# Kernel optimization log

Hardware: AMD Instinct MI355X
Metric: run time of the kernel (lower is better)

Reference implementation:

```python
import jax, jax.numpy as jnp
import numpy as np

N, B, PER, NELEM, E = 8192, 32, 256, 5, 131072
H, F, G, L = 128, 128, 50, 6
NC = B * NELEM
CUTOFF = 10.0
LOG2 = float(np.log(2.0))


def ssp(x):
    return jax.nn.softplus(x) - LOG2


def setup_inputs() -> dict:
    key = jax.random.key(0)
    ks = jax.random.split(key, 24)
    pos = jax.random.normal(ks[0], (N, 3), dtype=jnp.float32) * 2.0
    # component structure: node n in graph g gets element slot n % NELEM
    comp_id = (jnp.arange(N) // PER) * NELEM + (jnp.arange(N) % NELEM)
    comps_z = jax.random.randint(ks[1], (NC,), 1, 100)
    z = comps_z[comp_id]
    # edges restricted to within a graph (mimics radius_graph with batch)
    eg = jax.random.randint(ks[2], (E,), 0, B)
    src = eg * PER + jax.random.randint(ks[3], (E,), 0, PER)
    dst = eg * PER + jax.random.randint(ks[4], (E,), 0, PER)
    edge_index = jnp.stack([src, dst], axis=0)
    s = 0.05
    p = lambda k, shp: jax.random.normal(k, shp, dtype=jnp.float32) * s
    return {
        "pos": pos,
        "emb_table": p(ks[5], (100, H)),
        "mlp_w1": p(ks[6], (L, G, F)),
        "mlp_b1": jnp.zeros((L, F), jnp.float32),
        "mlp_w2": p(ks[7], (L, F, F)),
        "mlp_b2": jnp.zeros((L, F), jnp.float32),
        "cf_lin1_w": p(ks[8], (L, H, F)),
        "cf_lin2_w": p(ks[9], (L, F, H)),
        "cf_lin2_b": jnp.zeros((L, H), jnp.float32),
        "int_lin_w": p(ks[10], (L, H, H)),
        "int_lin_b": jnp.zeros((L, H), jnp.float32),
        "out_w1": p(ks[11], (H, H // 2)),
        "out_b1": jnp.zeros((H // 2,), jnp.float32),
        "out_w2": p(ks[12], (H // 2, 1)),
        "out_b2": jnp.zeros((1,), jnp.float32),
        "z": z,
        "comp_id": comp_id,
        "edge_index": edge_index,
        "comps_z": comps_z,
    }


def reference(pos, emb_table, mlp_w1, mlp_b1, mlp_w2, mlp_b2,
              cf_lin1_w, cf_lin2_w, cf_lin2_b, int_lin_w, int_lin_b,
              out_w1, out_b1, out_w2, out_b2,
              z, comp_id, edge_index, comps_z):
    src, dst = edge_index[0], edge_index[1]
    # edge distances and Gaussian smearing
    ew = jnp.linalg.norm(pos[src] - pos[dst], axis=-1)              # [E]
    offset = jnp.linspace(0.0, CUTOFF, G)
    coeff = -0.5 / (offset[1] - offset[0]) ** 2
    edge_attr = jnp.exp(coeff * (ew[:, None] - offset[None, :]) ** 2)  # [E,G]
    # cutoff envelope used by CFConv
    C = CUTOFF / (1e-10 + ew ** 2) - 1.0                            # [E]

    h = emb_table[z]                 # [N,H] node features (fixed across blocks)
    types = emb_table[comps_z]       # [NC,H] component features

    counts = jax.ops.segment_sum(jnp.ones((N,), jnp.float32), comp_id,
                                 num_segments=NC)                   # [NC]
    batch_c = jnp.arange(NC) // NELEM

    for i in range(L):
        # edge filter MLP * cutoff weight
        W = ssp(edge_attr @ mlp_w1[i] + mlp_b1[i]) @ mlp_w2[i] + mlp_b2[i]
        W = W * C[:, None]                                          # [E,F]
        xh = h @ cf_lin1_w[i]                                       # [N,F]
        msg = xh[src] * W                                           # [E,F]
        agg = jax.ops.segment_sum(msg, dst, num_segments=N)         # [N,F]
        # per-component mean pooling
        comp = jax.ops.segment_sum(agg, comp_id, num_segments=NC) / counts[:, None]
        x = comp @ cf_lin2_w[i] + cf_lin2_b[i]                      # [NC,H]
        x = ssp(x) @ int_lin_w[i] + int_lin_b[i]
        types = types + x

    # readout (num_tasks=1, n_seq=None branch)
    h2 = ssp(types @ out_w1 + out_b1)
    per_comp = h2 @ out_w2 + out_b2                                 # [NC,1]
    out = jax.ops.segment_sum(per_comp, batch_c, num_segments=B)    # [B,1]
    return out
```

## Files before the change

kernel.cpp:

```cpp
#include <hip/hip_runtime.h>


#define NNODES 8192
#define NGRAPH 32
#define NELEM  5
#define NEDGE  131072
#define HD     128
#define FD     128
#define GD     50
#define LL     6
#define NC     160
#define NZ     100
#define CUT    10.0f
#define LOG2_  0.69314718055994531f
#define LOG2E_ 1.44269504088896340f
#define QDC    0.84932181f

#define CAP    1024
#define PADE   (NC * CAP)
#define PADG   (PADE / 64)
#define GPITCH 72
#define TPITCH 136
#define CSTR   16

#define W1F_ELEMS (LL * 2 * 8 * 64 * 8)
#define W2F_ELEMS (LL * 4 * 8 * 64 * 8)
#define NSCATB   (NEDGE / 256)
#define NFRAGB   ((W1F_ELEMS + W2F_ELEMS) / 256)
#define NXHZB    (LL * NZ / 2)
#define NB2PB    3

typedef _Float16 half8 __attribute__((ext_vector_type(8)));
typedef float floatx4 __attribute__((ext_vector_type(4)));

#if __has_builtin(__builtin_amdgcn_exp2f)
#define EXP2F(x) __builtin_amdgcn_exp2f(x)
#else
#define EXP2F(x) __expf((x) * LOG2_)
#endif
#if __has_builtin(__builtin_amdgcn_logf)
#define LOG2F_(x) __builtin_amdgcn_logf(x)
#else
#define LOG2F_(x) (__logf(x) * LOG2E_)
#endif

__device__ __forceinline__ float ssp(float x) {
    float m = fmaxf(x, 0.0f);
    float z = __expf(-fabsf(x));
    return m + __logf(1.0f + z) - LOG2_;
}

__global__ __launch_bounds__(256) void setup_kernel(
    const float* __restrict__ pos, const int* __restrict__ ei,
    const int* __restrict__ comp_id, const int* __restrict__ z,
    const float* __restrict__ w1, const float* __restrict__ w2,
    const float* __restrict__ b2in,
    const float* __restrict__ emb, const float* __restrict__ cf1,
    int* __restrict__ counts, int* __restrict__ cursor,
    float* __restrict__ ew_s, float* __restrict__ c_s, int* __restrict__ zsrc_s,
    _Float16* __restrict__ w1f, _Float16* __restrict__ w2f,
    float* __restrict__ xh_z, float* __restrict__ b2p)
{
    int bx = blockIdx.x;
    int tid = threadIdx.x;
    if (bx < NSCATB) {
        int e = bx * 256 + tid;
        int s = ei[e], d = ei[NEDGE + e];
        float dx = pos[3*s]   - pos[3*d];
        float dy = pos[3*s+1] - pos[3*d+1];
        float dz = pos[3*s+2] - pos[3*d+2];
        float d2 = dx*dx + dy*dy + dz*dz;
        float ew = sqrtf(d2);
        float C  = CUT / (1e-10f + d2) - 1.0f;
        int cid = comp_id[d];
        int idx = cid * CAP + atomicAdd(&cursor[cid * CSTR], 1);
        ew_s[idx] = ew; c_s[idx] = C; zsrc_s[idx] = z[s];
        if (e < NNODES) atomicAdd(&counts[comp_id[e]], 1);
        return;
    }
    int fx = bx - NSCATB;
    if (fx < NFRAGB) {
        int idx = fx * 256 + tid;
        if (idx < W1F_ELEMS) {
            int j = idx & 7, lane = (idx >> 3) & 63, tcg = (idx >> 9) & 7;
            int kb = (idx >> 12) & 1, l = idx >> 13;
            int k = kb * 32 + (lane >> 4) * 8 + j;
            int col = tcg * 16 + (lane & 15);
            float v = (k < GD) ? w1[(l * GD + k) * FD + col] : 0.0f;
            w1f[idx] = (_Float16)(v * LOG2E_);
        } else {
            int id2 = idx - W1F_ELEMS;
            int j = id2 & 7, lane = (id2 >> 3) & 63, tcg = (id2 >> 9) & 7;
            int kb = (id2 >> 12) & 3, l = id2 >> 14;
            int k = kb * 32 + (lane >> 4) * 8 + j;
            int col = tcg * 16 + (lane & 15);
            w2f[id2] = (_Float16)(LOG2_ * w2[(l * FD + k) * FD + col]);
        }
        return;
    }
    int bz = fx - NFRAGB;
    if (bz < NXHZB) {
        int l = bz / (NZ / 2);
        int zv = (bz % (NZ / 2)) * 2 + (tid >> 7);
        int f = tid & 127;
        const float* h = emb + zv * HD;
        const float* w = cf1 + l * HD * FD;
        float acc = 0.0f;
        #pragma unroll 8
        for (int k = 0; k < HD; ++k) acc = fmaf(h[k], w[k * FD + f], acc);
        xh_z[(l * NZ + zv) * FD + f] = acc;
    } else {
        int idx2 = (bz - NXHZB) * 256 + tid;
        int l = idx2 >> 7, fo = idx2 & 127;
        float sum = 0.0f;
        #pragma unroll 8
        for (int fi = 0; fi < FD; ++fi)
            sum += (float)(_Float16)(LOG2_ * w2[(l * FD + fi) * FD + fo]);
        b2p[idx2] = b2in[l * FD + fo] - sum;
    }
}

__global__ __launch_bounds__(256, 8) void edge_kernel(
    const float* __restrict__ ew_s, const float* __restrict__ c_s,
    const int* __restrict__ zsrc_s,
    const _Float16* __restrict__ w1f, const float* __restrict__ b1_,
    const _Float16* __restrict__ w2f, const float* __restrict__ b2p_,
    const float* __restrict__ xh_z, float* __restrict__ comp_acc)
{
    __shared__ __align__(16) _Float16 smem[64 * TPITCH];
    __shared__ float ce_l[64];
    __shared__ int   zs_l[64];

    const int tid  = threadIdx.x;
    const int lane = tid & 63;
    const int l15  = lane & 15;
    const int quad = lane >> 4;
    const int fq   = __builtin_amdgcn_readfirstlane(tid >> 6);
    const int l    = blockIdx.y;
    const int cid  = blockIdx.x % NC;
    const int gg   = blockIdx.x / NC;
    const int g0   = cid * CAP + gg * 64;

    const float delta = CUT / (GD - 1);
    const float Qe = QDC / delta;

    const float ce = c_s[g0 + lane];
    if (__all(ce == 0.0f)) return;
    if (tid < 64) {
        ce_l[tid] = ce;
        zs_l[tid] = zsrc_s[g0 + tid] * (FD * 4);
    }
    const int colbase = fq * 32 + l15;
    const float b1c0 = b1_[l * FD + colbase] * LOG2E_;
    const float b1c1 = b1_[l * FD + colbase + 16] * LOG2E_;
    const float b2c0 = b2p_[l * FD + colbase];
    const float b2c1 = b2p_[l * FD + colbase + 16];

    {
        const float qewr = ew_s[g0 + lane] * Qe;
        half8 ga, gb;
        #pragma unroll
        for (int i = 0; i < 8; ++i) {
            float u0 = qewr - (fq * 16 + i) * QDC;
            float u1 = qewr - (fq * 16 + 8 + i) * QDC;
            ga[i] = (_Float16)EXP2F(-(u0 * u0));
            gb[i] = (_Float16)EXP2F(-(u1 * u1));
        }
        *(half8*)&smem[lane * GPITCH + fq * 16]     = ga;
        *(half8*)&smem[lane * GPITCH + fq * 16 + 8] = gb;
    }
    __syncthreads();

    floatx4 accT[4][2];
    #pragma unroll
    for (int tr = 0; tr < 4; ++tr) {
        accT[tr][0] = (floatx4){b1c0, b1c0, b1c0, b1c0};
        accT[tr][1] = (floatx4){b1c1, b1c1, b1c1, b1c1};
    }
    const half8* w1fp = (const half8*)w1f;
    #pragma unroll
    for (int kb = 0; kb < 2; ++kb) {
        half8 bf0 = w1fp[((l * 2 + kb) * 8 + fq * 2 + 0) * 64 + lane];
        half8 bf1 = w1fp[((l * 2 + kb) * 8 + fq * 2 + 1) * 64 + lane];
        #pragma unroll
        for (int tr = 0; tr < 4; ++tr) {
            half8 af = *(const half8*)&smem[(tr * 16 + l15) * GPITCH + kb * 32 + quad * 8];
            accT[tr][0] = __builtin_amdgcn_mfma_f32_16x16x32_f16(af, bf0, accT[tr][0], 0, 0, 0);
            accT[tr][1] = __builtin_amdgcn_mfma_f32_16x16x32_f16(af, bf1, accT[tr][1], 0, 0, 0);
        }
    }
    __syncthreads();

    #pragma unroll
    for (int tr = 0; tr < 4; ++tr) {
        #pragma unroll
        for (int tcl = 0; tcl < 2; ++tcl) {
            #pragma unroll
            for (int r = 0; r < 4; ++r) {
                float ee = EXP2F(accT[tr][tcl][r]);
                smem[(tr * 16 + quad * 4 + r) * TPITCH + fq * 32 + tcl * 16 + l15]
                    = (_Float16)LOG2F_(1.0f + ee);
            }
        }
    }
    __syncthreads();

    floatx4 accW[4][2];
    #pragma unroll
    for (int tr = 0; tr < 4; ++tr) {
        accW[tr][0] = (floatx4){b2c0, b2c0, b2c0, b2c0};
        accW[tr][1] = (floatx4){b2c1, b2c1, b2c1, b2c1};
    }
    const half8* w2fp = (const half8*)w2f;
    #pragma unroll
    for (int kb = 0; kb < 4; ++kb) {
        half8 bf0 = w2fp[((l * 4 + kb) * 8 + fq * 2 + 0) * 64 + lane];
        half8 bf1 = w2fp[((l * 4 + kb) * 8 + fq * 2 + 1) * 64 + lane];
        #pragma unroll
        for (int tr = 0; tr < 4; ++tr) {
            half8 af = *(const half8*)&smem[(tr * 16 + l15) * TPITCH + kb * 32 + quad * 8];
            accW[tr][0] = __builtin_amdgcn_mfma_f32_16x16x32_f16(af, bf0, accW[tr][0], 0, 0, 0);
            accW[tr][1] = __builtin_amdgcn_mfma_f32_16x16x32_f16(af, bf1, accW[tr][1], 0, 0, 0);
        }
    }

    const char* xb = (const char*)(xh_z + l * NZ * FD) + colbase * 4;
    float s0 = 0.0f, s1 = 0.0f;
    #pragma unroll
    for (int tr = 0; tr < 4; ++tr) {
        #pragma unroll
        for (int r = 0; r < 4; ++r) {
            const int e = tr * 16 + quad * 4 + r;
            const float cee = ce_l[e];
            const float* xr = (const float*)(xb + zs_l[e]);
            float p0 = cee * xr[0];
            float p1 = cee * xr[16];
            s0 = fmaf(accW[tr][0][r], p0, s0);
            s1 = fmaf(accW[tr][1][r], p1, s1);
        }
    }
    s0 += __shfl_xor(s0, 16); s0 += __shfl_xor(s0, 32);
    s1 += __shfl_xor(s1, 16); s1 += __shfl_xor(s1, 32);
    float* cacc = comp_acc + (l * NC + cid) * FD + fq * 32;
    if (quad == 0) {
        atomicAdd(&cacc[l15],      s0);
        atomicAdd(&cacc[l15 + 16], s1);
    }
}

__global__ __launch_bounds__(128) void comp_kernel(
    const float* __restrict__ comp_acc, const int* __restrict__ counts,
    const float* __restrict__ cf2w, const float* __restrict__ cf2b,
    const float* __restrict__ intw, const float* __restrict__ intb,
    float* __restrict__ types_acc)
{
    int c = blockIdx.x, l = blockIdx.y, f = threadIdx.x;
    __shared__ float comp[FD];
    __shared__ float sx[FD];
    comp[f] = comp_acc[(l * NC + c) * FD + f] / (float)counts[c];
    __syncthreads();
    float acc = cf2b[l * HD + f];
    const float* w = cf2w + l * FD * HD;
    #pragma unroll 8
    for (int k = 0; k < FD; ++k) acc = fmaf(comp[k], w[k * HD + f], acc);
    sx[f] = ssp(acc);
    __syncthreads();
    float acc2 = intb[l * HD + f];
    const float* wi = intw + l * HD * HD;
    #pragma unroll 8
    for (int k = 0; k < HD; ++k) acc2 = fmaf(sx[k], wi[k * HD + f], acc2);
    atomicAdd(&types_acc[c * HD + f], acc2);
}

__global__ __launch_bounds__(64) void readout_kernel(
    const float* __restrict__ types_acc, const float* __restrict__ emb,
    const int* __restrict__ comps_z,
    const float* __restrict__ w1, const float* __restrict__ b1,
    const float* __restrict__ w2, const float* __restrict__ b2,
    float* __restrict__ out)
{
    int b = blockIdx.x, lane = threadIdx.x;
    float sum = 0.0f;
    for (int cc = 0; cc < NELEM; ++cc) {
        int c = b * NELEM + cc;
        int zc = comps_z[c];
        float acc = b1[lane];
        const float* ta = types_acc + c * HD;
        const float* eb = emb + zc * HD;
        #pragma unroll 8
        for (int k = 0; k < HD; ++k) acc = fmaf(ta[k] + eb[k], w1[k * 64 + lane], acc);
        sum += ssp(acc) * w2[lane];
    }
    #pragma unroll
    for (int s = 32; s > 0; s >>= 1) sum += __shfl_xor(sum, s);
    if (lane == 0) out[b] = sum + (float)NELEM * b2[0];
}

extern "C" void kernel_launch(void* const* d_in, const int* in_sizes, int n_in,
                              void* d_out, int out_size, void* d_ws, size_t ws_size,
                              hipStream_t stream) {
    (void)in_sizes; (void)n_in; (void)out_size; (void)ws_size;
    const float* pos     = (const float*)d_in[0];
    const float* emb     = (const float*)d_in[1];
    const float* mlp_w1  = (const float*)d_in[2];
    const float* mlp_b1  = (const float*)d_in[3];
    const float* mlp_w2  = (const float*)d_in[4];
    const float* mlp_b2  = (const float*)d_in[5];
    const float* cf1     = (const float*)d_in[6];
    const float* cf2w    = (const float*)d_in[7];
    const float* cf2b    = (const float*)d_in[8];
    const float* intw    = (const float*)d_in[9];
    const float* intb    = (const float*)d_in[10];
    const float* ow1     = (const float*)d_in[11];
    const float* ob1     = (const float*)d_in[12];
    const float* ow2     = (const float*)d_in[13];
    const float* ob2     = (const float*)d_in[14];
    const int*   z       = (const int*)d_in[15];
    const int*   comp_id = (const int*)d_in[16];
    const int*   ei      = (const int*)d_in[17];
    const int*   comps_z = (const int*)d_in[18];
    float* out = (float*)d_out;

    char* ws = (char*)d_ws;
    size_t off = 0;
    auto alloc = [&](size_t bytes) -> void* {
        void* p = ws + off;
        off += (bytes + 255) & ~(size_t)255;
        return p;
    };
    float* comp_acc  = (float*)alloc((size_t)LL * NC * FD * 4);
    int*   counts    = (int*)  alloc(NC * 4);
    float* types_acc = (float*)alloc((size_t)NC * HD * 4);
    int*   cursor    = (int*)  alloc(NC * CSTR * 4);
    float* c_s       = (float*)alloc((size_t)PADE * 4);
    int*   zsrc_s    = (int*)  alloc((size_t)PADE * 4);
    size_t zero_bytes = off;
    float* ew_s     = (float*)alloc((size_t)PADE * 4);
    float* xh_z     = (float*)alloc((size_t)LL * NZ * FD * 4);
    float* b2p      = (float*)alloc((size_t)LL * FD * 4);
    _Float16* w1f   = (_Float16*)alloc((size_t)W1F_ELEMS * 2);
    _Float16* w2f   = (_Float16*)alloc((size_t)W2F_ELEMS * 2);

    hipMemsetAsync(d_ws, 0, zero_bytes, stream);

    setup_kernel<<<NSCATB + NFRAGB + NXHZB + NB2PB, 256, 0, stream>>>(
        pos, ei, comp_id, z, mlp_w1, mlp_w2, mlp_b2, emb, cf1,
        counts, cursor, ew_s, c_s, zsrc_s, w1f, w2f, xh_z, b2p);
    edge_kernel <<<dim3(PADG, LL), 256, 0, stream>>>(ew_s, c_s, zsrc_s,
                                                     w1f, mlp_b1, w2f, b2p,
                                                     xh_z, comp_acc);
    comp_kernel <<<dim3(NC, LL), 128, 0, stream>>>(comp_acc, counts, cf2w, cf2b,
                                                   intw, intb, types_acc);
    readout_kernel<<<NGRAPH, 64, 0, stream>>>(types_acc, emb, comps_z,
                                              ow1, ob1, ow2, ob2, out);
}
```

Measured before the change: 212.1 us.

## Process three layers per edge block, swizzle LDS, and pack xh_z pairs

Each edge_kernel block now loops over three layers instead of one, so the grid's y dimension drops from 6 to 2. The Gaussian smearing, the early-exit check and the per-edge metadata loads are shared across those layers. The LDS writes and reads of the hidden activations are XOR-swizzled to reduce bank conflicts. xh_z columns are permuted in setup so each lane can fetch its two features with one float2 load, and ce/zsrc are packed into one int2 in LDS. ew_s is moved into the zeroed region, which adds memset work, and the lower occupancy hint plus fewer blocks reduce the parallelism available to hide latency.

Measured after the change: 224.7 us. +5.9%, slower.

```diff
diff --git a/kernel.cpp b/kernel.cpp
--- a/kernel.cpp
+++ b/kernel.cpp
@@ -108,7 +108,8 @@
         float acc = 0.0f;
         #pragma unroll 8
         for (int k = 0; k < HD; ++k) acc = fmaf(h[k], w[k * FD + f], acc);
-        xh_z[(l * NZ + zv) * FD + f] = acc;
+        int fp = ((f >> 5) * 32) + ((f & 15) * 2) + ((f >> 4) & 1);
+        xh_z[(l * NZ + zv) * FD + fp] = acc;
     } else {
         int idx2 = (bz - NXHZB) * 256 + tid;
         int l = idx2 >> 7, fo = idx2 & 127;
@@ -120,7 +121,7 @@
     }
 }
 
-__global__ __launch_bounds__(256, 8) void edge_kernel(
+__global__ __launch_bounds__(256, 6) void edge_kernel(
     const float* __restrict__ ew_s, const float* __restrict__ c_s,
     const int* __restrict__ zsrc_s,
     const _Float16* __restrict__ w1f, const float* __restrict__ b1_,
@@ -128,37 +129,28 @@
     const float* __restrict__ xh_z, float* __restrict__ comp_acc)
 {
     __shared__ __align__(16) _Float16 smem[64 * TPITCH];
-    __shared__ float ce_l[64];
-    __shared__ int   zs_l[64];
+    __shared__ int2 cz_l[64];
 
     const int tid  = threadIdx.x;
     const int lane = tid & 63;
     const int l15  = lane & 15;
     const int quad = lane >> 4;
     const int fq   = __builtin_amdgcn_readfirstlane(tid >> 6);
-    const int l    = blockIdx.y;
     const int cid  = blockIdx.x % NC;
     const int gg   = blockIdx.x / NC;
     const int g0   = cid * CAP + gg * 64;
+    const int l0   = blockIdx.y * 3;
+
+    const float ce = c_s[g0 + lane];
+    if (__all(ce == 0.0f)) return;
+    if (tid < 64)
+        cz_l[tid] = make_int2(__float_as_int(ce), zsrc_s[g0 + tid] * (FD * 4));
 
     const float delta = CUT / (GD - 1);
     const float Qe = QDC / delta;
-
-    const float ce = c_s[g0 + lane];
-    if (__all(ce == 0.0f)) return;
-    if (tid < 64) {
-        ce_l[tid] = ce;
-        zs_l[tid] = zsrc_s[g0 + tid] * (FD * 4);
-    }
-    const int colbase = fq * 32 + l15;
-    const float b1c0 = b1_[l * FD + colbase] * LOG2E_;
-    const float b1c1 = b1_[l * FD + colbase + 16] * LOG2E_;
-    const float b2c0 = b2p_[l * FD + colbase];
-    const float b2c1 = b2p_[l * FD + colbase + 16];
-
+    half8 ga, gb;
     {
         const float qewr = ew_s[g0 + lane] * Qe;
-        half8 ga, gb;
         #pragma unroll
         for (int i = 0; i < 8; ++i) {
             float u0 = qewr - (fq * 16 + i) * QDC;
@@ -166,85 +158,101 @@
             ga[i] = (_Float16)EXP2F(-(u0 * u0));
             gb[i] = (_Float16)EXP2F(-(u1 * u1));
         }
+    }
+    const int colbase = fq * 32 + l15;
+    const int wsw = quad << 4;
+    const int rsw = ((l15 >> 2) & 3) << 4;
+
+    #pragma unroll 1
+    for (int li = 0; li < 3; ++li) {
+        const int l = l0 + li;
+
         *(half8*)&smem[lane * GPITCH + fq * 16]     = ga;
         *(half8*)&smem[lane * GPITCH + fq * 16 + 8] = gb;
-    }
-    __syncthreads();
-
-    floatx4 accT[4][2];
-    #pragma unroll
-    for (int tr = 0; tr < 4; ++tr) {
-        accT[tr][0] = (floatx4){b1c0, b1c0, b1c0, b1c0};
-        accT[tr][1] = (floatx4){b1c1, b1c1, b1c1, b1c1};
-    }
-    const half8* w1fp = (const half8*)w1f;
-    #pragma unroll
-    for (int kb = 0; kb < 2; ++kb) {
-        half8 bf0 = w1fp[((l * 2 + kb) * 8 + fq * 2 + 0) * 64 + lane];
-        half8 bf1 = w1fp[((l * 2 + kb) * 8 + fq * 2 + 1) * 64 + lane];
+        const float b1c0 = b1_[l * FD + colbase] * LOG2E_;
+        const float b1c1 = b1_[l * FD + colbase + 16] * LOG2E_;
+        const float b2c0 = b2p_[l * FD + colbase];
+        const float b2c1 = b2p_[l * FD + colbase + 16];
+        __syncthreads();
+
+        floatx4 accT[4][2];
         #pragma unroll
         for (int tr = 0; tr < 4; ++tr) {
-            half8 af = *(const half8*)&smem[(tr * 16 + l15) * GPITCH + kb * 32 + quad * 8];
-            accT[tr][0] = __builtin_amdgcn_mfma_f32_16x16x32_f16(af, bf0, accT[tr][0], 0, 0, 0);
-            accT[tr][1] = __builtin_amdgcn_mfma_f32_16x16x32_f16(af, bf1, accT[tr][1], 0, 0, 0);
-        }
-    }
-    __syncthreads();
-
-    #pragma unroll
-    for (int tr = 0; tr < 4; ++tr) {
-        #pragma unroll
-        for (int tcl = 0; tcl < 2; ++tcl) {
+            accT[tr][0] = (floatx4){b1c0, b1c0, b1c0, b1c0};
+            accT[tr][1] = (floatx4){b1c1, b1c1, b1c1, b1c1};
+        }
+        const half8* w1fp = (const half8*)w1f;
+        #pragma unroll
+        for (int kb = 0; kb < 2; ++kb) {
+            half8 bf0 = w1fp[((l * 2 + kb) * 8 + fq * 2 + 0) * 64 + lane];
+            half8 bf1 = w1fp[((l * 2 + kb) * 8 + fq * 2 + 1) * 64 + lane];
+            #pragma unroll
+            for (int tr = 0; tr < 4; ++tr) {
+                half8 af = *(const half8*)&smem[(tr * 16 + l15) * GPITCH + kb * 32 + quad * 8];
+                accT[tr][0] = __builtin_amdgcn_mfma_f32_16x16x32_f16(af, bf0, accT[tr][0], 0, 0, 0);
+                accT[tr][1] = __builtin_amdgcn_mfma_f32_16x16x32_f16(af, bf1, accT[tr][1], 0, 0, 0);
+            }
+        }
+        __syncthreads();
+
+        #pragma unroll
+        for (int tr = 0; tr < 4; ++tr) {
+            #pragma unroll
+            for (int tcl = 0; tcl < 2; ++tcl) {
+                #pragma unroll
+                for (int r = 0; r < 4; ++r) {
+                    float ee = EXP2F(accT[tr][tcl][r]);
+                    smem[(tr * 16 + quad * 4 + r) * TPITCH
+                         + ((fq * 32 + tcl * 16 + l15) ^ wsw)]
+                        = (_Float16)LOG2F_(1.0f + ee);
+                }
+            }
+        }
+        __syncthreads();
+
+        floatx4 accW[4][2];
+        #pragma unroll
+        for (int tr = 0; tr < 4; ++tr) {
+            accW[tr][0] = (floatx4){b2c0, b2c0, b2c0, b2c0};
+            accW[tr][1] = (floatx4){b2c1, b2c1, b2c1, b2c1};
+        }
+        const half8* w2fp = (const half8*)w2f;
+        #pragma unroll
+        for (int kb = 0; kb < 4; ++kb) {
+            half8 bf0 = w2fp[((l * 4 + kb) * 8 + fq * 2 + 0) * 64 + lane];
+            half8 bf1 = w2fp[((l * 4 + kb) * 8 + fq * 2 + 1) * 64 + lane];
+            #pragma unroll
+            for (int tr = 0; tr < 4; ++tr) {
+                half8 af = *(const half8*)&smem[(tr * 16 + l15) * TPITCH
+                                                + ((kb * 32 + quad * 8) ^ rsw)];
+                accW[tr][0] = __builtin_amdgcn_mfma_f32_16x16x32_f16(af, bf0, accW[tr][0], 0, 0, 0);
+                accW[tr][1] = __builtin_amdgcn_mfma_f32_16x16x32_f16(af, bf1, accW[tr][1], 0, 0, 0);
+            }
+        }
+
+        const char* xb = (const char*)xh_z
+                       + ((size_t)(l * NZ * FD) + (size_t)(fq * 32 + l15 * 2)) * 4;
+        float s0 = 0.0f, s1 = 0.0f;
+        #pragma unroll
+        for (int tr = 0; tr < 4; ++tr) {
             #pragma unroll
             for (int r = 0; r < 4; ++r) {
-                float ee = EXP2F(accT[tr][tcl][r]);
-                smem[(tr * 16 + quad * 4 + r) * TPITCH + fq * 32 + tcl * 16 + l15]
-                    = (_Float16)LOG2F_(1.0f + ee);
+                const int e = tr * 16 + quad * 4 + r;
+                int2 cz = cz_l[e];
+                float cee = __int_as_float(cz.x);
+                const float2 xr = *(const float2*)(xb + cz.y);
+                s0 = fmaf(accW[tr][0][r], cee * xr.x, s0);
+                s1 = fmaf(accW[tr][1][r], cee * xr.y, s1);
             }
         }
-    }
-    __syncthreads();
-
-    floatx4 accW[4][2];
-    #pragma unroll
-    for (int tr = 0; tr < 4; ++tr) {
-        accW[tr][0] = (floatx4){b2c0, b2c0, b2c0, b2c0};
-        accW[tr][1] = (floatx4){b2c1, b2c1, b2c1, b2c1};
-    }
-    const half8* w2fp = (const half8*)w2f;
-    #pragma unroll
-    for (int kb = 0; kb < 4; ++kb) {
-        half8 bf0 = w2fp[((l * 4 + kb) * 8 + fq * 2 + 0) * 64 + lane];
-        half8 bf1 = w2fp[((l * 4 + kb) * 8 + fq * 2 + 1) * 64 + lane];
-        #pragma unroll
-        for (int tr = 0; tr < 4; ++tr) {
-            half8 af = *(const half8*)&smem[(tr * 16 + l15) * TPITCH + kb * 32 + quad * 8];
-            accW[tr][0] = __builtin_amdgcn_mfma_f32_16x16x32_f16(af, bf0, accW[tr][0], 0, 0, 0);
-            accW[tr][1] = __builtin_amdgcn_mfma_f32_16x16x32_f16(af, bf1, accW[tr][1], 0, 0, 0);
-        }
-    }
-
-    const char* xb = (const char*)(xh_z + l * NZ * FD) + colbase * 4;
-    float s0 = 0.0f, s1 = 0.0f;
-    #pragma unroll
-    for (int tr = 0; tr < 4; ++tr) {
-        #pragma unroll
-        for (int r = 0; r < 4; ++r) {
-            const int e = tr * 16 + quad * 4 + r;
-            const float cee = ce_l[e];
-            const float* xr = (const float*)(xb + zs_l[e]);
-            float p0 = cee * xr[0];
-            float p1 = cee * xr[16];
-            s0 = fmaf(accW[tr][0][r], p0, s0);
-            s1 = fmaf(accW[tr][1][r], p1, s1);
-        }
-    }
-    s0 += __shfl_xor(s0, 16); s0 += __shfl_xor(s0, 32);
-    s1 += __shfl_xor(s1, 16); s1 += __shfl_xor(s1, 32);
-    float* cacc = comp_acc + (l * NC + cid) * FD + fq * 32;
-    if (quad == 0) {
-        atomicAdd(&cacc[l15],      s0);
-        atomicAdd(&cacc[l15 + 16], s1);
+        s0 += __shfl_xor(s0, 16); s0 += __shfl_xor(s0, 32);
+        s1 += __shfl_xor(s1, 16); s1 += __shfl_xor(s1, 32);
+        float* cacc = comp_acc + (l * NC + cid) * FD + fq * 32;
+        if (quad == 0) {
+            atomicAdd(&cacc[l15],      s0);
+            atomicAdd(&cacc[l15 + 16], s1);
+        }
+        if (li < 2) __syncthreads();
     }
 }
 
@@ -334,8 +342,8 @@
     int*   cursor    = (int*)  alloc(NC * CSTR * 4);
     float* c_s       = (float*)alloc((size_t)PADE * 4);
     int*   zsrc_s    = (int*)  alloc((size_t)PADE * 4);
+    float* ew_s      = (float*)alloc((size_t)PADE * 4);
     size_t zero_bytes = off;
-    float* ew_s     = (float*)alloc((size_t)PADE * 4);
     float* xh_z     = (float*)alloc((size_t)LL * NZ * FD * 4);
     float* b2p      = (float*)alloc((size_t)LL * FD * 4);
     _Float16* w1f   = (_Float16*)alloc((size_t)W1F_ELEMS * 2);
@@ -346,9 +354,9 @@
     setup_kernel<<<NSCATB + NFRAGB + NXHZB + NB2PB, 256, 0, stream>>>(
         pos, ei, comp_id, z, mlp_w1, mlp_w2, mlp_b2, emb, cf1,
         counts, cursor, ew_s, c_s, zsrc_s, w1f, w2f, xh_z, b2p);
-    edge_kernel <<<dim3(PADG, LL), 256, 0, stream>>>(ew_s, c_s, zsrc_s,
-                                                     w1f, mlp_b1, w2f, b2p,
-                                                     xh_z, comp_acc);
+    edge_kernel <<<dim3(PADG, 2), 256, 0, stream>>>(ew_s, c_s, zsrc_s,
+                                                    w1f, mlp_b1, w2f, b2p,
+                                                    xh_z, comp_acc);
     comp_kernel <<<dim3(NC, LL), 128, 0, stream>>>(comp_acc, counts, cf2w, cf2b,
                                                    intw, intb, types_acc);
     readout_kernel<<<NGRAPH, 64, 0, stream>>>(types_acc, emb, comps_z,
```

## Replace per-edge filter MLP with interpolated distance lookup table

Applied to the files above, without the earlier changes.

The filter network depends only on the scalar edge distance, so it is evaluated once per layer on a 2048-point distance grid in the setup kernel and stored as an fp16 table. The edge kernel then linearly interpolates table rows instead of running two MFMA matmuls per edge. It also handles all six layers in one block, sharing edge metadata and issuing fewer launches. The trade-off is interpolation and fp16 error, plus clamping of distances beyond the table range (about 12.8).

Measured after the change: 273.6 us. 1.29x slower.

```diff
diff --git a/kernel.cpp b/kernel.cpp
--- a/kernel.cpp
+++ b/kernel.cpp
@@ -13,54 +13,43 @@
 #define NZ     100
 #define CUT    10.0f
 #define LOG2_  0.69314718055994531f
-#define LOG2E_ 1.44269504088896340f
-#define QDC    0.84932181f
 
 #define CAP    1024
 #define PADE   (NC * CAP)
 #define PADG   (PADE / 64)
-#define GPITCH 72
-#define TPITCH 136
 #define CSTR   16
 
-#define W1F_ELEMS (LL * 2 * 8 * 64 * 8)
-#define W2F_ELEMS (LL * 4 * 8 * 64 * 8)
-#define NSCATB   (NEDGE / 256)
-#define NFRAGB   ((W1F_ELEMS + W2F_ELEMS) / 256)
-#define NXHZB    (LL * NZ / 2)
-#define NB2PB    3
-
-typedef _Float16 half8 __attribute__((ext_vector_type(8)));
-typedef float floatx4 __attribute__((ext_vector_type(4)));
-
-#if __has_builtin(__builtin_amdgcn_exp2f)
-#define EXP2F(x) __builtin_amdgcn_exp2f(x)
-#else
-#define EXP2F(x) __expf((x) * LOG2_)
-#endif
-#if __has_builtin(__builtin_amdgcn_logf)
-#define LOG2F_(x) __builtin_amdgcn_logf(x)
-#else
-#define LOG2F_(x) (__logf(x) * LOG2E_)
-#endif
+#define NK     2048
+#define TI     32
+#define HSTEP  0.00625f
+#define INVH   160.0f
+#define DELTA  (10.0f / 49.0f)
+#define COEFF  (-12.005f)
+
+#define NSCATB (NEDGE / 256)
+#define NXHZB  (LL * NZ / 2)
+#define NTABB  (LL * (NK / TI))
+
+typedef _Float16 h2 __attribute__((ext_vector_type(2)));
 
 __device__ __forceinline__ float ssp(float x) {
     float m = fmaxf(x, 0.0f);
-    float z = __expf(-fabsf(x));
-    return m + __logf(1.0f + z) - LOG2_;
+    float zz = __expf(-fabsf(x));
+    return m + __logf(1.0f + zz) - LOG2_;
 }
 
 __global__ __launch_bounds__(256) void setup_kernel(
     const float* __restrict__ pos, const int* __restrict__ ei,
     const int* __restrict__ comp_id, const int* __restrict__ z,
-    const float* __restrict__ w1, const float* __restrict__ w2,
-    const float* __restrict__ b2in,
+    const float* __restrict__ w1, const float* __restrict__ b1in,
+    const float* __restrict__ w2, const float* __restrict__ b2in,
     const float* __restrict__ emb, const float* __restrict__ cf1,
     int* __restrict__ counts, int* __restrict__ cursor,
     float* __restrict__ ew_s, float* __restrict__ c_s, int* __restrict__ zsrc_s,
-    _Float16* __restrict__ w1f, _Float16* __restrict__ w2f,
-    float* __restrict__ xh_z, float* __restrict__ b2p)
-{
+    _Float16* __restrict__ xh16, _Float16* __restrict__ tab)
+{
+    __shared__ float Gl[TI][52];
+    __shared__ float Sl[TI][FD];
     int bx = blockIdx.x;
     int tid = threadIdx.x;
     if (bx < NSCATB) {
@@ -78,27 +67,7 @@
         if (e < NNODES) atomicAdd(&counts[comp_id[e]], 1);
         return;
     }
-    int fx = bx - NSCATB;
-    if (fx < NFRAGB) {
-        int idx = fx * 256 + tid;
-        if (idx < W1F_ELEMS) {
-            int j = idx & 7, lane = (idx >> 3) & 63, tcg = (idx >> 9) & 7;
-            int kb = (idx >> 12) & 1, l = idx >> 13;
-            int k = kb * 32 + (lane >> 4) * 8 + j;
-            int col = tcg * 16 + (lane & 15);
-            float v = (k < GD) ? w1[(l * GD + k) * FD + col] : 0.0f;
-            w1f[idx] = (_Float16)(v * LOG2E_);
-        } else {
-            int id2 = idx - W1F_ELEMS;
-            int j = id2 & 7, lane = (id2 >> 3) & 63, tcg = (id2 >> 9) & 7;
-            int kb = (id2 >> 12) & 3, l = id2 >> 14;
-            int k = kb * 32 + (lane >> 4) * 8 + j;
-            int col = tcg * 16 + (lane & 15);
-            w2f[id2] = (_Float16)(LOG2_ * w2[(l * FD + k) * FD + col]);
-        }
-        return;
-    }
-    int bz = fx - NFRAGB;
+    int bz = bx - NSCATB;
     if (bz < NXHZB) {
         int l = bz / (NZ / 2);
         int zv = (bz % (NZ / 2)) * 2 + (tid >> 7);
@@ -108,143 +77,111 @@
         float acc = 0.0f;
         #pragma unroll 8
         for (int k = 0; k < HD; ++k) acc = fmaf(h[k], w[k * FD + f], acc);
-        xh_z[(l * NZ + zv) * FD + f] = acc;
-    } else {
-        int idx2 = (bz - NXHZB) * 256 + tid;
-        int l = idx2 >> 7, fo = idx2 & 127;
-        float sum = 0.0f;
-        #pragma unroll 8
-        for (int fi = 0; fi < FD; ++fi)
-            sum += (float)(_Float16)(LOG2_ * w2[(l * FD + fi) * FD + fo]);
-        b2p[idx2] = b2in[l * FD + fo] - sum;
+        xh16[(l * NZ + zv) * FD + f] = (_Float16)acc;
+        return;
+    }
+    int bt = bz - NXHZB;
+    int l  = bt >> 6;
+    int i0 = (bt & 63) * TI;
+    for (int idx = tid; idx < TI * GD; idx += 256) {
+        int il = idx / GD, k = idx - il * GD;
+        float d = (float)(i0 + il) * HSTEP - (float)k * DELTA;
+        Gl[il][k] = __expf(COEFF * d * d);
+    }
+    __syncthreads();
+    {
+        int f = tid & 127;
+        float b1v = b1in[l * FD + f];
+        #pragma unroll 1
+        for (int it = 0; it < TI / 2; ++it) {
+            int il = (tid >> 7) + it * 2;
+            float t = b1v;
+            #pragma unroll 10
+            for (int k = 0; k < GD; ++k)
+                t = fmaf(Gl[il][k], w1[(l * GD + k) * FD + f], t);
+            Sl[il][f] = ssp(t);
+        }
+    }
+    __syncthreads();
+    {
+        int f = tid & 127;
+        float b2v = b2in[l * FD + f];
+        #pragma unroll 1
+        for (int it = 0; it < TI / 2; ++it) {
+            int il = (tid >> 7) + it * 2;
+            float wv = b2v;
+            #pragma unroll 8
+            for (int k = 0; k < FD; ++k)
+                wv = fmaf(Sl[il][k], w2[(l * FD + k) * FD + f], wv);
+            tab[((size_t)(l * NK + i0 + il)) * FD + f] = (_Float16)wv;
+        }
     }
 }
 
 __global__ __launch_bounds__(256, 8) void edge_kernel(
     const float* __restrict__ ew_s, const float* __restrict__ c_s,
     const int* __restrict__ zsrc_s,
-    const _Float16* __restrict__ w1f, const float* __restrict__ b1_,
-    const _Float16* __restrict__ w2f, const float* __restrict__ b2p_,
-    const float* __restrict__ xh_z, float* __restrict__ comp_acc)
-{
-    __shared__ __align__(16) _Float16 smem[64 * TPITCH];
-    __shared__ float ce_l[64];
-    __shared__ int   zs_l[64];
+    const _Float16* __restrict__ tab, const _Float16* __restrict__ xh16,
+    float* __restrict__ comp_acc)
+{
+    __shared__ int4 meta[64];
 
     const int tid  = threadIdx.x;
     const int lane = tid & 63;
-    const int l15  = lane & 15;
-    const int quad = lane >> 4;
-    const int fq   = __builtin_amdgcn_readfirstlane(tid >> 6);
-    const int l    = blockIdx.y;
+    const int fq   = tid >> 6;
     const int cid  = blockIdx.x % NC;
     const int gg   = blockIdx.x / NC;
     const int g0   = cid * CAP + gg * 64;
 
-    const float delta = CUT / (GD - 1);
-    const float Qe = QDC / delta;
-
     const float ce = c_s[g0 + lane];
     if (__all(ce == 0.0f)) return;
+
     if (tid < 64) {
-        ce_l[tid] = ce;
-        zs_l[tid] = zsrc_s[g0 + tid] * (FD * 4);
-    }
-    const int colbase = fq * 32 + l15;
-    const float b1c0 = b1_[l * FD + colbase] * LOG2E_;
-    const float b1c1 = b1_[l * FD + colbase + 16] * LOG2E_;
-    const float b2c0 = b2p_[l * FD + colbase];
-    const float b2c1 = b2p_[l * FD + colbase + 16];
-
-    {
-        const float qewr = ew_s[g0 + lane] * Qe;
-        half8 ga, gb;
+        float ew = ew_s[g0 + tid];
+        int zz   = zsrc_s[g0 + tid];
+        float fi = ew * INVH;
+        int i = (int)fi; if (i > NK - 2) i = NK - 2;
+        float fr = fi - (float)i; if (fr > 1.0f) fr = 1.0f;
+        meta[tid] = make_int4(i * (FD * 2), __float_as_int(fr),
+                              __float_as_int(c_s[g0 + tid]), zz * (FD * 2));
+    }
+    __syncthreads();
+
+    float acc[LL][2];
+    #pragma unroll
+    for (int l = 0; l < LL; ++l) { acc[l][0] = 0.0f; acc[l][1] = 0.0f; }
+
+    const int lane4 = lane * 4;
+    for (int k = 0; k < 16; ++k) {
+        int4 m = meta[fq * 16 + k];
+        const int   ib = __builtin_amdgcn_readfirstlane(m.x);
+        const float fr = __int_as_float(__builtin_amdgcn_readfirstlane(m.y));
+        const float C  = __int_as_float(__builtin_amdgcn_readfirstlane(m.z));
+        const int   xo = __builtin_amdgcn_readfirstlane(m.w);
+        const _Float16 frh = (_Float16)fr;
+        const h2 fr2 = {frh, frh};
         #pragma unroll
-        for (int i = 0; i < 8; ++i) {
-            float u0 = qewr - (fq * 16 + i) * QDC;
-            float u1 = qewr - (fq * 16 + 8 + i) * QDC;
-            ga[i] = (_Float16)EXP2F(-(u0 * u0));
-            gb[i] = (_Float16)EXP2F(-(u1 * u1));
+        for (int l = 0; l < LL; ++l) {
+            const char* tp = (const char*)tab  + (size_t)l * (NK * FD * 2) + ib;
+            const char* xp = (const char*)xh16 + (size_t)l * (NZ * FD * 2) + xo;
+            unsigned ua = *(const unsigned*)(tp + lane4);
+            unsigned ub = *(const unsigned*)(tp + lane4 + FD * 2);
+            unsigned ux = *(const unsigned*)(xp + lane4);
+            h2 a2 = __builtin_bit_cast(h2, ua);
+            h2 b2 = __builtin_bit_cast(h2, ub);
+            h2 x2 = __builtin_bit_cast(h2, ux);
+            h2 w2v = fr2 * (b2 - a2) + a2;
+            float x0 = (float)x2[0], x1 = (float)x2[1];
+            acc[l][0] = fmaf((float)w2v[0], C * x0, acc[l][0]);
+            acc[l][1] = fmaf((float)w2v[1], C * x1, acc[l][1]);
         }
-        *(half8*)&smem[lane * GPITCH + fq * 16]     = ga;
-        *(half8*)&smem[lane * GPITCH + fq * 16 + 8] = gb;
-    }
-    __syncthreads();
-
-    floatx4 accT[4][2];
+    }
+
+    float* cacc = comp_acc + cid * FD + lane * 2;
     #pragma unroll
-    for (int tr = 0; tr < 4; ++tr) {
-        accT[tr][0] = (floatx4){b1c0, b1c0, b1c0, b1c0};
-        accT[tr][1] = (floatx4){b1c1, b1c1, b1c1, b1c1};
-    }
-    const half8* w1fp = (const half8*)w1f;
-    #pragma unroll
-    for (int kb = 0; kb < 2; ++kb) {
-        half8 bf0 = w1fp[((l * 2 + kb) * 8 + fq * 2 + 0) * 64 + lane];
-        half8 bf1 = w1fp[((l * 2 + kb) * 8 + fq * 2 + 1) * 64 + lane];
-        #pragma unroll
-        for (int tr = 0; tr < 4; ++tr) {
-            half8 af = *(const half8*)&smem[(tr * 16 + l15) * GPITCH + kb * 32 + quad * 8];
-            accT[tr][0] = __builtin_amdgcn_mfma_f32_16x16x32_f16(af, bf0, accT[tr][0], 0, 0, 0);
-            accT[tr][1] = __builtin_amdgcn_mfma_f32_16x16x32_f16(af, bf1, accT[tr][1], 0, 0, 0);
-        }
-    }
-    __syncthreads();
-
-    #pragma unroll
-    for (int tr = 0; tr < 4; ++tr) {
-        #pragma unroll
-        for (int tcl = 0; tcl < 2; ++tcl) {
-            #pragma unroll
-            for (int r = 0; r < 4; ++r) {
-                float ee = EXP2F(accT[tr][tcl][r]);
-                smem[(tr * 16 + quad * 4 + r) * TPITCH + fq * 32 + tcl * 16 + l15]
-                    = (_Float16)LOG2F_(1.0f + ee);
-            }
-        }
-    }
-    __syncthreads();
-
-    floatx4 accW[4][2];
-    #pragma unroll
-    for (int tr = 0; tr < 4; ++tr) {
-        accW[tr][0] = (floatx4){b2c0, b2c0, b2c0, b2c0};
-        accW[tr][1] = (floatx4){b2c1, b2c1, b2c1, b2c1};
-    }
-    const half8* w2fp = (const half8*)w2f;
-    #pragma unroll
-    for (int kb = 0; kb < 4; ++kb) {
-        half8 bf0 = w2fp[((l * 4 + kb) * 8 + fq * 2 + 0) * 64 + lane];
-        half8 bf1 = w2fp[((l * 4 + kb) * 8 + fq * 2 + 1) * 64 + lane];
-        #pragma unroll
-        for (int tr = 0; tr < 4; ++tr) {
-            half8 af = *(const half8*)&smem[(tr * 16 + l15) * TPITCH + kb * 32 + quad * 8];
-            accW[tr][0] = __builtin_amdgcn_mfma_f32_16x16x32_f16(af, bf0, accW[tr][0], 0, 0, 0);
-            accW[tr][1] = __builtin_amdgcn_mfma_f32_16x16x32_f16(af, bf1, accW[tr][1], 0, 0, 0);
-        }
-    }
-
-    const char* xb = (const char*)(xh_z + l * NZ * FD) + colbase * 4;
-    float s0 = 0.0f, s1 = 0.0f;
-    #pragma unroll
-    for (int tr = 0; tr < 4; ++tr) {
-        #pragma unroll
-        for (int r = 0; r < 4; ++r) {
-            const int e = tr * 16 + quad * 4 + r;
-            const float cee = ce_l[e];
-            const float* xr = (const float*)(xb + zs_l[e]);
-            float p0 = cee * xr[0];
-            float p1 = cee * xr[16];
-            s0 = fmaf(accW[tr][0][r], p0, s0);
-            s1 = fmaf(accW[tr][1][r], p1, s1);
-        }
-    }
-    s0 += __shfl_xor(s0, 16); s0 += __shfl_xor(s0, 32);
-    s1 += __shfl_xor(s1, 16); s1 += __shfl_xor(s1, 32);
-    float* cacc = comp_acc + (l * NC + cid) * FD + fq * 32;
-    if (quad == 0) {
-        atomicAdd(&cacc[l15],      s0);
-        atomicAdd(&cacc[l15 + 16], s1);
+    for (int l = 0; l < LL; ++l) {
+        atomicAdd(&cacc[l * NC * FD],     acc[l][0]);
+        atomicAdd(&cacc[l * NC * FD + 1], acc[l][1]);
     }
 }
 
@@ -334,21 +271,17 @@
     int*   cursor    = (int*)  alloc(NC * CSTR * 4);
     float* c_s       = (float*)alloc((size_t)PADE * 4);
     int*   zsrc_s    = (int*)  alloc((size_t)PADE * 4);
+    float* ew_s      = (float*)alloc((size_t)PADE * 4);
     size_t zero_bytes = off;
-    float* ew_s     = (float*)alloc((size_t)PADE * 4);
-    float* xh_z     = (float*)alloc((size_t)LL * NZ * FD * 4);
-    float* b2p      = (float*)alloc((size_t)LL * FD * 4);
-    _Float16* w1f   = (_Float16*)alloc((size_t)W1F_ELEMS * 2);
-    _Float16* w2f   = (_Float16*)alloc((size_t)W2F_ELEMS * 2);
-
-    hipMemsetAsync(d_ws, 0, zero_bytes, stream);
-
-    setup_kernel<<<NSCATB + NFRAGB + NXHZB + NB2PB, 256, 0, stream>>>(
-        pos, ei, comp_id, z, mlp_w1, mlp_w2, mlp_b2, emb, cf1,
-        counts, cursor, ew_s, c_s, zsrc_s, w1f, w2f, xh_z, b2p);
-    edge_kernel <<<dim3(PADG, LL), 256, 0, stream>>>(ew_s, c_s, zsrc_s,
-                                                     w1f, mlp_b1, w2f, b2p,
-                                                     xh_z, comp_acc);
+    _Float16* xh16 = (_Float16*)alloc((size_t)LL * NZ * FD * 2);
+    _Float16* tab  = (_Float16*)alloc((size_t)LL * NK * FD * 2);
+
+    (void)hipMemsetAsync(d_ws, 0, zero_bytes, stream);
+
+    setup_kernel<<<NSCATB + NXHZB + NTABB, 256, 0, stream>>>(
+        pos, ei, comp_id, z, mlp_w1, mlp_b1, mlp_w2, mlp_b2, emb, cf1,
+        counts, cursor, ew_s, c_s, zsrc_s, xh16, tab);
+    edge_kernel <<<PADG, 256, 0, stream>>>(ew_s, c_s, zsrc_s, tab, xh16, comp_acc);
     comp_kernel <<<dim3(NC, LL), 128, 0, stream>>>(comp_acc, counts, cf2w, cf2b,
                                                    intw, intb, types_acc);
     readout_kernel<<<NGRAPH, 64, 0, stream>>>(types_acc, emb, comps_z,
```
